# Performance work log

Measured on AMD Instinct MI355X. Metric: run time of the kernel, lower is better.

## Reference

```python
import jax, jax.numpy as jnp
import numpy as np

N_NODES = 50000
N_EDGES = 800000
D_IN = 256
D_HID = 256
D_OUT = 8


def _glorot(key, shape):
    fan_in = shape[-1]
    bound = 1.0 / np.sqrt(fan_in)
    return jax.random.uniform(key, shape, minval=-bound, maxval=bound, dtype=jnp.float32)


def setup_inputs() -> dict:
    key = jax.random.key(0)
    ks = jax.random.split(key, 12)
    x = jax.random.normal(ks[0], (N_NODES, D_IN), dtype=jnp.float32)
    edge_index = jax.random.randint(ks[1], (2, N_EDGES), 0, N_NODES, dtype=jnp.int64)
    return {
        "x": x,
        "edge_index": edge_index,
        # SAGEConv1: lin_l (neighbor path, has bias), lin_r (root path, no bias)
        "W1l": _glorot(ks[2], (D_HID, D_IN)),
        "b1": jnp.zeros((D_HID,), jnp.float32),
        "W1r": _glorot(ks[3], (D_HID, D_IN)),
        # SAGEConv2
        "W2l": _glorot(ks[4], (D_HID, D_HID)),
        "b2": jnp.zeros((D_HID,), jnp.float32),
        "W2r": _glorot(ks[5], (D_HID, D_HID)),
        # MLP decoder
        "Wm1": _glorot(ks[6], (D_HID, D_HID)),
        "bm1": _glorot(ks[7], (D_HID,)),
        "Wm2": _glorot(ks[8], (D_OUT, D_HID)),
        "bm2": _glorot(ks[9], (D_OUT,)),
    }


def _sage_conv(x, edge_index, Wl, b, Wr):
    # PyG SAGEConv with mean aggregation:
    # out = lin_l(mean_{j in N(i)} x_j) + lin_r(x_i)
    src, dst = edge_index[0], edge_index[1]
    msg = x[src]  # [E, d] gather
    agg = jax.ops.segment_sum(msg, dst, num_segments=x.shape[0])  # [N, d]
    cnt = jax.ops.segment_sum(jnp.ones((edge_index.shape[1],), x.dtype), dst,
                              num_segments=x.shape[0])  # in-degree [N]
    mean = agg / jnp.maximum(cnt, 1.0)[:, None]
    return mean @ Wl.T + b + x @ Wr.T


def reference(x, edge_index, W1l, b1, W1r, W2l, b2, W2r, Wm1, bm1, Wm2, bm2):
    h = jax.nn.relu(_sage_conv(x, edge_index, W1l, b1, W1r))
    h = jax.nn.relu(_sage_conv(h, edge_index, W2l, b2, W2r))
    h = jax.nn.relu(h @ Wm1.T + bm1)
    logits = h @ Wm2.T + bm2
    return jax.nn.softmax(logits, axis=-1)
```

## Files before the change

### kernel.cpp

```cpp
#include <hip/hip_runtime.h>
#include <math.h>

#define N_NODES 50000
#define N_EDGES 800000
#define D 256

typedef unsigned short u16;
typedef __attribute__((ext_vector_type(8))) __bf16 bf16x8;
typedef __attribute__((ext_vector_type(4))) float f32x4;

#define BUF_U16 24576
#define NBUF 3

__device__ __forceinline__ void split_hi_lo(float v, u16& h, u16& l) {
    unsigned u = __float_as_uint(v);
    unsigned hh = (u + 0x7fff + ((u >> 16) & 1)) >> 16;
    float hf = __uint_as_float(hh << 16);
    float res = v - hf;
    unsigned ul = __float_as_uint(res);
    unsigned ll = (ul + 0x7fff + ((ul >> 16) & 1)) >> 16;
    h = (u16)hh; l = (u16)ll;
}

__device__ __forceinline__ float bflo(unsigned u) { return __uint_as_float(u << 16); }
__device__ __forceinline__ float bfhi(unsigned u) { return __uint_as_float(u & 0xffff0000u); }

__device__ __forceinline__ void gl_lds16(const void* g, void* l) {
    __builtin_amdgcn_global_load_lds(
        (const __attribute__((address_space(1))) void*)g,
        (__attribute__((address_space(3))) void*)l, 16, 0, 0);
}

__global__ void zero_i32(int* __restrict__ p, int n) {
    int i = blockIdx.x * blockDim.x + threadIdx.x;
    if (i < n) p[i] = 0;
}

__global__ void count_deg(const int* __restrict__ ei, int* __restrict__ cnt) {
    int e = blockIdx.x * blockDim.x + threadIdx.x;
    if (e < N_EDGES) atomicAdd(&cnt[ei[N_EDGES + e]], 1);
}

__global__ void scan1(const int* __restrict__ cnt, int* __restrict__ partial,
                      int* __restrict__ bsum) {
    __shared__ int s[1024];
    int t = threadIdx.x, b = blockIdx.x;
    int gid = b * 1024 + t;
    int v = (gid < N_NODES) ? cnt[gid] : 0;
    s[t] = v;
    __syncthreads();
    for (int off = 1; off < 1024; off <<= 1) {
        int u = (t >= off) ? s[t - off] : 0;
        __syncthreads();
        s[t] += u;
        __syncthreads();
    }
    partial[gid] = s[t];
    if (t == 1023) bsum[b] = s[1023];
}

__global__ void scan2(const int* __restrict__ bsum, int* __restrict__ boff, int nb) {
    int t = threadIdx.x;
    int orig = (t < nb) ? bsum[t] : 0;
    int v = orig;
    #pragma unroll
    for (int off = 1; off < 64; off <<= 1) {
        int u = __shfl_up(v, off, 64);
        if (t >= off) v += u;
    }
    boff[t] = v - orig;
}

__global__ void scan3(const int* __restrict__ partial, const int* __restrict__ boff,
                      int* __restrict__ rowptr, int* __restrict__ cursor) {
    int i = blockIdx.x * blockDim.x + threadIdx.x;
    if (i <= N_NODES) {
        int val = 0;
        if (i > 0) val = partial[i - 1] + boff[(i - 1) >> 10];
        rowptr[i] = val;
        if (i < N_NODES) cursor[i] = val;
    }
}

__global__ void fill_edges(const int* __restrict__ ei, int* __restrict__ cursor,
                           int* __restrict__ esrc) {
    int e = blockIdx.x * blockDim.x + threadIdx.x;
    if (e < N_EDGES) {
        int p = atomicAdd(&cursor[ei[N_EDGES + e]], 1);
        esrc[p] = ei[e];
    }
}

__global__ void split_bf16(const float* __restrict__ in, u16* __restrict__ hi,
                           u16* __restrict__ lo, int n) {
    int i = blockIdx.x * blockDim.x + threadIdx.x;
    if (i < n) {
        u16 h, l; split_hi_lo(in[i], h, l);
        hi[i] = h; lo[i] = l;
    }
}

__global__ __launch_bounds__(256) void aggregate_bf16(const u16* __restrict__ in_hi,
        const int* __restrict__ rowptr, const int* __restrict__ esrc,
        u16* __restrict__ ohi, u16* __restrict__ olo) {
    int node = blockIdx.x * 4 + (threadIdx.x >> 6);
    if (node >= N_NODES) return;
    int lane = threadIdx.x & 63;
    int half = lane >> 5;
    int sub = lane & 31;
    int beg = rowptr[node], end = rowptr[node + 1];
    const u16* rowp = in_hi + sub * 8;

    float a0 = 0.f, a1 = 0.f, a2 = 0.f, a3 = 0.f;
    float a4 = 0.f, a5 = 0.f, a6 = 0.f, a7 = 0.f;

#define ACC8(v) \
    a0 += bflo(v.x); a1 += bfhi(v.x); a2 += bflo(v.y); a3 += bfhi(v.y); \
    a4 += bflo(v.z); a5 += bfhi(v.z); a6 += bflo(v.w); a7 += bfhi(v.w);

    int j = beg;
    for (; j + 16 <= end; j += 16) {
        int i0 = esrc[j +  0 + half];
        int i1 = esrc[j +  2 + half];
        int i2 = esrc[j +  4 + half];
        int i3 = esrc[j +  6 + half];
        int i4 = esrc[j +  8 + half];
        int i5 = esrc[j + 10 + half];
        int i6 = esrc[j + 12 + half];
        int i7 = esrc[j + 14 + half];
        uint4 r0 = *(const uint4*)(rowp + (size_t)i0 * D);
        uint4 r1 = *(const uint4*)(rowp + (size_t)i1 * D);
        uint4 r2 = *(const uint4*)(rowp + (size_t)i2 * D);
        uint4 r3 = *(const uint4*)(rowp + (size_t)i3 * D);
        uint4 r4 = *(const uint4*)(rowp + (size_t)i4 * D);
        uint4 r5 = *(const uint4*)(rowp + (size_t)i5 * D);
        uint4 r6 = *(const uint4*)(rowp + (size_t)i6 * D);
        uint4 r7 = *(const uint4*)(rowp + (size_t)i7 * D);
        ACC8(r0); ACC8(r1); ACC8(r2); ACC8(r3);
        ACC8(r4); ACC8(r5); ACC8(r6); ACC8(r7);
    }
    for (; j + 8 <= end; j += 8) {
        int i0 = esrc[j + 0 + half];
        int i1 = esrc[j + 2 + half];
        int i2 = esrc[j + 4 + half];
        int i3 = esrc[j + 6 + half];
        uint4 r0 = *(const uint4*)(rowp + (size_t)i0 * D);
        uint4 r1 = *(const uint4*)(rowp + (size_t)i1 * D);
        uint4 r2 = *(const uint4*)(rowp + (size_t)i2 * D);
        uint4 r3 = *(const uint4*)(rowp + (size_t)i3 * D);
        ACC8(r0); ACC8(r1); ACC8(r2); ACC8(r3);
    }
    for (; j < end; j += 2) {
        int e = j + half;
        if (e < end) {
            uint4 r = *(const uint4*)(rowp + (size_t)esrc[e] * D);
            ACC8(r);
        }
    }
#undef ACC8

    a0 += __shfl_xor(a0, 32, 64); a1 += __shfl_xor(a1, 32, 64);
    a2 += __shfl_xor(a2, 32, 64); a3 += __shfl_xor(a3, 32, 64);
    a4 += __shfl_xor(a4, 32, 64); a5 += __shfl_xor(a5, 32, 64);
    a6 += __shfl_xor(a6, 32, 64); a7 += __shfl_xor(a7, 32, 64);

    if (lane < 32) {
        float inv = 1.f / (float)max(end - beg, 1);
        float m[8] = { a0 * inv, a1 * inv, a2 * inv, a3 * inv,
                       a4 * inv, a5 * inv, a6 * inv, a7 * inv };
        u16 h[8], l[8];
        #pragma unroll
        for (int k = 0; k < 8; ++k) split_hi_lo(m[k], h[k], l[k]);
        size_t o = (size_t)node * D + lane * 8;
        *(uint4*)(ohi + o) = make_uint4(h[0] | (h[1] << 16), h[2] | (h[3] << 16),
                                        h[4] | (h[5] << 16), h[6] | (h[7] << 16));
        *(uint4*)(olo + o) = make_uint4(l[0] | (l[1] << 16), l[2] | (l[3] << 16),
                                        l[4] | (l[5] << 16), l[6] | (l[7] << 16));
    }
}

__device__ __forceinline__ void stage256(u16* buf,
        const u16* __restrict__ Ah, const u16* __restrict__ Al,
        const u16* __restrict__ Bh, const u16* __restrict__ Bl,
        int ks, int m0, int n0, int t) {
    int tr = t >> 2;
    int g  = (t & 3) ^ ((t >> 3) & 3);
    size_t boff = (size_t)(n0 + tr) * D + ks + g * 8;
    gl_lds16(Bh + boff, buf + 16384 + t * 8);
    gl_lds16(Bl + boff, buf + 20480 + t * 8);
    #pragma unroll
    for (int r = 0; r < 2; ++r) {
        int arow = m0 + r * 128 + tr; if (arow >= N_NODES) arow = N_NODES - 1;
        size_t aoff = (size_t)arow * D + ks + g * 8;
        gl_lds16(Ah + aoff, buf + r * 4096 + t * 8);
        gl_lds16(Al + aoff, buf + 8192 + r * 4096 + t * 8);
    }
}

__global__ __launch_bounds__(512, 1) void gemm_mfma(
        const u16* __restrict__ A1h, const u16* __restrict__ A1l,
        const u16* __restrict__ A2h, const u16* __restrict__ A2l,
        const u16* __restrict__ B1h, const u16* __restrict__ B1l,
        const u16* __restrict__ B2h, const u16* __restrict__ B2l,
        const float* __restrict__ bias, int K, int relu,
        float* __restrict__ Cf, u16* __restrict__ Chi, u16* __restrict__ Clo) {
    extern __shared__ u16 sh[];
    const int t = threadIdx.x;
    const int lane = t & 63;
    const int w = t >> 6;
    const int wm = (w >> 1) * 64, wn = (w & 1) * 64;

    int bid = blockIdx.x;
    int m_idx, n_idx;
    if (bid < 384) {
        m_idx = (bid >> 4) * 8 + (bid & 7);
        n_idx = (bid >> 3) & 1;
    } else {
        int r = bid - 384;
        m_idx = 192 + (r & 3);
        n_idx = r >> 2;
    }
    const int m0 = m_idx * 256, n0 = n_idx * 128;

    f32x4 acc[4][4] = {};

    const int lm = lane & 15;
    const int sw = ((lane >> 4) ^ ((lm >> 1) & 3)) * 8;
    const int nsteps = K >> 5;

    stage256(sh,           A1h, A1l, B1h, B1l,  0, m0, n0, t);
    stage256(sh + BUF_U16, A1h, A1l, B1h, B1l, 32, m0, n0, t);

    int cur = 0;
    for (int s = 0; s < nsteps; ++s) {
        if (s + 1 < nsteps) {
            asm volatile("s_waitcnt vmcnt(6)" ::: "memory");
        } else {
            asm volatile("s_waitcnt vmcnt(0)" ::: "memory");
        }
        __builtin_amdgcn_s_barrier();
        __builtin_amdgcn_sched_barrier(0);

        if (s + 2 < nsteps) {
            int sb = cur + 2; if (sb >= NBUF) sb -= NBUF;
            int ksg = (s + 2) * 32;
            if (ksg < 256) stage256(sh + sb * BUF_U16, A1h, A1l, B1h, B1l, ksg,       m0, n0, t);
            else           stage256(sh + sb * BUF_U16, A2h, A2l, B2h, B2l, ksg - 256, m0, n0, t);
        }

        const u16* buf = sh + cur * BUF_U16;
        bf16x8 ah[4], al[4], bh[4], bl[4];
        #pragma unroll
        for (int i = 0; i < 4; ++i) {
            int offA = (wm + i * 16 + lm) * 32 + sw;
            ah[i] = *(const bf16x8*)(buf + offA);
            al[i] = *(const bf16x8*)(buf + 8192 + offA);
            int offB = (wn + i * 16 + lm) * 32 + sw;
            bh[i] = *(const bf16x8*)(buf + 16384 + offB);
            bl[i] = *(const bf16x8*)(buf + 20480 + offB);
        }
        __builtin_amdgcn_s_setprio(1);
        #pragma unroll
        for (int i = 0; i < 4; ++i) {
            #pragma unroll
            for (int j = 0; j < 4; ++j) {
                acc[i][j] = __builtin_amdgcn_mfma_f32_16x16x32_bf16(ah[i], bh[j], acc[i][j], 0, 0, 0);
                acc[i][j] = __builtin_amdgcn_mfma_f32_16x16x32_bf16(ah[i], bl[j], acc[i][j], 0, 0, 0);
                acc[i][j] = __builtin_amdgcn_mfma_f32_16x16x32_bf16(al[i], bh[j], acc[i][j], 0, 0, 0);
            }
        }
        __builtin_amdgcn_s_setprio(0);

        cur = (cur == NBUF - 1) ? 0 : cur + 1;
    }

    const int q = lane >> 4;
    #pragma unroll
    for (int j = 0; j < 4; ++j) {
        int col = n0 + wn + j * 16 + lm;
        float bb = bias[col];
        #pragma unroll
        for (int i = 0; i < 4; ++i) {
            int rowb = m0 + wm + i * 16 + q * 4;
            #pragma unroll
            for (int r = 0; r < 4; ++r) {
                int row = rowb + r;
                if (row < N_NODES) {
                    float v = acc[i][j][r] + bb;
                    if (relu) v = fmaxf(v, 0.f);
                    size_t o = (size_t)row * D + col;
                    if (Cf) Cf[o] = v;
                    if (Chi) {
                        u16 h, l; split_hi_lo(v, h, l);
                        Chi[o] = h; Clo[o] = l;
                    }
                }
            }
        }
    }
}

__global__ __launch_bounds__(256) void mlp2_softmax(const float* __restrict__ h,
        const float* __restrict__ W, const float* __restrict__ b,
        float* __restrict__ out) {
    int wid = threadIdx.x >> 6;
    int lane = threadIdx.x & 63;
    int n = blockIdx.x * 4 + wid;
    if (n >= N_NODES) return;

    float4 hv = ((const float4*)(h + (size_t)n * D))[lane];
    float acc[8];
    #pragma unroll
    for (int o = 0; o < 8; ++o) {
        float4 w = ((const float4*)(W + o * D))[lane];
        acc[o] = hv.x * w.x + hv.y * w.y + hv.z * w.z + hv.w * w.w;
    }
    #pragma unroll
    for (int o = 0; o < 8; ++o) {
        #pragma unroll
        for (int off = 32; off >= 1; off >>= 1)
            acc[o] += __shfl_xor(acc[o], off, 64);
    }
    if (lane == 0) {
        float v[8];
        float m = -1e30f;
        #pragma unroll
        for (int o = 0; o < 8; ++o) { v[o] = acc[o] + b[o]; m = fmaxf(m, v[o]); }
        float s = 0.f;
        #pragma unroll
        for (int o = 0; o < 8; ++o) { v[o] = expf(v[o] - m); s += v[o]; }
        float inv = 1.f / s;
        float4 o0 = make_float4(v[0] * inv, v[1] * inv, v[2] * inv, v[3] * inv);
        float4 o1 = make_float4(v[4] * inv, v[5] * inv, v[6] * inv, v[7] * inv);
        ((float4*)(out + (size_t)n * 8))[0] = o0;
        ((float4*)(out + (size_t)n * 8))[1] = o1;
    }
}

static inline size_t align_up(size_t x) { return (x + 255) & ~(size_t)255; }

extern "C" void kernel_launch(void* const* d_in, const int* in_sizes, int n_in,
                              void* d_out, int out_size, void* d_ws, size_t ws_size,
                              hipStream_t stream) {
    const float* x   = (const float*)d_in[0];
    const int*   ei  = (const int*)d_in[1];
    const float* W1l = (const float*)d_in[2];
    const float* b1  = (const float*)d_in[3];
    const float* W1r = (const float*)d_in[4];
    const float* W2l = (const float*)d_in[5];
    const float* b2  = (const float*)d_in[6];
    const float* W2r = (const float*)d_in[7];
    const float* Wm1 = (const float*)d_in[8];
    const float* bm1 = (const float*)d_in[9];
    const float* Wm2 = (const float*)d_in[10];
    const float* bm2 = (const float*)d_in[11];
    float* out = (float*)d_out;

    const size_t NF = (size_t)N_NODES * D;
    const size_t NW = (size_t)D * D;

    char* w = (char*)d_ws;
    u16* x_hi  = (u16*)w; w += align_up(NF * 2);
    u16* x_lo  = (u16*)w; w += align_up(NF * 2);
    u16* mn_hi = (u16*)w; w += align_up(NF * 2 * 2);
    u16* mn_lo = mn_hi + NF;
    u16* h1_hi = (u16*)w; w += align_up(NF * 2);
    u16* h1_lo = (u16*)w; w += align_up(NF * 2);
    u16* h2_hi = (u16*)w; w += align_up(NF * 2);
    u16* h2_lo = (u16*)w; w += align_up(NF * 2);
    u16* wbuf  = (u16*)w; w += align_up(NW * 2 * 10);
    u16* w1l_h = wbuf + 0 * NW; u16* w1l_l = wbuf + 1 * NW;
    u16* w1r_h = wbuf + 2 * NW; u16* w1r_l = wbuf + 3 * NW;
    u16* w2l_h = wbuf + 4 * NW; u16* w2l_l = wbuf + 5 * NW;
    u16* w2r_h = wbuf + 6 * NW; u16* w2r_l = wbuf + 7 * NW;
    u16* wm1_h = wbuf + 8 * NW; u16* wm1_l = wbuf + 9 * NW;
    int* cnt     = (int*)w; w += align_up((size_t)N_NODES * 4);
    int* rowptr  = (int*)w; w += align_up((size_t)(N_NODES + 1) * 4);
    int* cursor  = (int*)w; w += align_up((size_t)N_NODES * 4);
    int* partial = (int*)w; w += align_up((size_t)49 * 1024 * 4);
    int* bsum    = (int*)w; w += align_up((size_t)64 * 4);
    int* boff    = (int*)w; w += align_up((size_t)64 * 4);
    int* esrc    = (int*)w; w += align_up((size_t)N_EDGES * 4);
    float* h3 = (float*)mn_hi;

    static bool attr_done = false;
    if (!attr_done) {
        hipFuncSetAttribute((const void*)gemm_mfma,
                            hipFuncAttributeMaxDynamicSharedMemorySize,
                            NBUF * BUF_U16 * 2);
        attr_done = true;
    }

    zero_i32<<<(N_NODES + 255) / 256, 256, 0, stream>>>(cnt, N_NODES);
    count_deg<<<(N_EDGES + 255) / 256, 256, 0, stream>>>(ei, cnt);
    scan1<<<49, 1024, 0, stream>>>(cnt, partial, bsum);
    scan2<<<1, 64, 0, stream>>>(bsum, boff, 49);
    scan3<<<(N_NODES + 256) / 256, 256, 0, stream>>>(partial, boff, rowptr, cursor);
    fill_edges<<<(N_EDGES + 255) / 256, 256, 0, stream>>>(ei, cursor, esrc);

    split_bf16<<<(int)((NF + 255) / 256), 256, 0, stream>>>(x, x_hi, x_lo, (int)NF);
    split_bf16<<<(int)((NW + 255) / 256), 256, 0, stream>>>(W1l, w1l_h, w1l_l, (int)NW);
    split_bf16<<<(int)((NW + 255) / 256), 256, 0, stream>>>(W1r, w1r_h, w1r_l, (int)NW);
    split_bf16<<<(int)((NW + 255) / 256), 256, 0, stream>>>(W2l, w2l_h, w2l_l, (int)NW);
    split_bf16<<<(int)((NW + 255) / 256), 256, 0, stream>>>(W2r, w2r_h, w2r_l, (int)NW);
    split_bf16<<<(int)((NW + 255) / 256), 256, 0, stream>>>(Wm1, wm1_h, wm1_l, (int)NW);

    const int GEMM_LDS = NBUF * BUF_U16 * 2;
    dim3 ggrid(392);
    int agrid = (N_NODES + 3) / 4;

    aggregate_bf16<<<agrid, 256, 0, stream>>>(x_hi, rowptr, esrc, mn_hi, mn_lo);
    gemm_mfma<<<ggrid, 512, GEMM_LDS, stream>>>(mn_hi, mn_lo, x_hi, x_lo,
                                                w1l_h, w1l_l, w1r_h, w1r_l,
                                                b1, 512, 1, nullptr, h1_hi, h1_lo);
    aggregate_bf16<<<agrid, 256, 0, stream>>>(h1_hi, rowptr, esrc, mn_hi, mn_lo);
    gemm_mfma<<<ggrid, 512, GEMM_LDS, stream>>>(mn_hi, mn_lo, h1_hi, h1_lo,
                                                w2l_h, w2l_l, w2r_h, w2r_l,
                                                b2, 512, 1, nullptr, h2_hi, h2_lo);
    gemm_mfma<<<ggrid, 512, GEMM_LDS, stream>>>(h2_hi, h2_lo, h2_hi, h2_lo,
                                                wm1_h, wm1_l, wm1_h, wm1_l,
                                                bm1, 256, 1, h3, nullptr, nullptr);
    mlp2_softmax<<<(N_NODES + 3) / 4, 256, 0, stream>>>(h3, Wm2, bm2, out);
}
```

Measured before the change: 551.0 us.

## Fuse MLP hidden GEMM with output layer and softmax; stage GEMM epilogue through LDS

Replaces the third gemm_mfma launch plus the separate mlp2_softmax kernel with one gemm_mlp2 kernel. It computes a 128x256 tile of the hidden layer, keeps it in LDS, then does the 8-wide output projection and softmax in the same block. This removes the fp32 h3 round trip through global memory and one launch. The conv GEMM epilogue now also writes hi/lo results to LDS first and stores them as coalesced 16-byte vectors instead of scattered 2-byte stores. The cost is an extra barrier and an LDS pass, plus a new kernel that covers full N per block, with fewer blocks (391) and one block per CU.

Result: faster. 519.4 us (-5.7%).

```diff
diff --git a/kernel.cpp b/kernel.cpp
--- a/kernel.cpp
+++ b/kernel.cpp
@@ -202,8 +202,8 @@
         const u16* __restrict__ A2h, const u16* __restrict__ A2l,
         const u16* __restrict__ B1h, const u16* __restrict__ B1l,
         const u16* __restrict__ B2h, const u16* __restrict__ B2l,
-        const float* __restrict__ bias, int K, int relu,
-        float* __restrict__ Cf, u16* __restrict__ Chi, u16* __restrict__ Clo) {
+        const float* __restrict__ bias, int K,
+        u16* __restrict__ Chi, u16* __restrict__ Clo) {
     extern __shared__ u16 sh[];
     const int t = threadIdx.x;
     const int lane = t & 63;
@@ -274,66 +274,168 @@
         cur = (cur == NBUF - 1) ? 0 : cur + 1;
     }
 
+    __syncthreads();
     const int q = lane >> 4;
     #pragma unroll
     for (int j = 0; j < 4; ++j) {
-        int col = n0 + wn + j * 16 + lm;
-        float bb = bias[col];
+        int col = wn + j * 16 + lm;
+        float bb = bias[n0 + col];
         #pragma unroll
         for (int i = 0; i < 4; ++i) {
-            int rowb = m0 + wm + i * 16 + q * 4;
             #pragma unroll
             for (int r = 0; r < 4; ++r) {
-                int row = rowb + r;
-                if (row < N_NODES) {
-                    float v = acc[i][j][r] + bb;
-                    if (relu) v = fmaxf(v, 0.f);
-                    size_t o = (size_t)row * D + col;
-                    if (Cf) Cf[o] = v;
-                    if (Chi) {
-                        u16 h, l; split_hi_lo(v, h, l);
-                        Chi[o] = h; Clo[o] = l;
-                    }
-                }
+                int row = wm + i * 16 + q * 4 + r;
+                float v = fmaxf(acc[i][j][r] + bb, 0.f);
+                u16 h, l; split_hi_lo(v, h, l);
+                sh[row * 128 + col] = h;
+                sh[32768 + row * 128 + col] = l;
             }
         }
     }
-}
-
-__global__ __launch_bounds__(256) void mlp2_softmax(const float* __restrict__ h,
-        const float* __restrict__ W, const float* __restrict__ b,
-        float* __restrict__ out) {
-    int wid = threadIdx.x >> 6;
-    int lane = threadIdx.x & 63;
-    int n = blockIdx.x * 4 + wid;
-    if (n >= N_NODES) return;
-
-    float4 hv = ((const float4*)(h + (size_t)n * D))[lane];
-    float acc[8];
+    __syncthreads();
+    for (int c = t; c < 4096; c += 512) {
+        int row = c >> 4;
+        int off = (c & 15) * 8;
+        int grow = m0 + row;
+        if (grow < N_NODES) {
+            size_t o = (size_t)grow * D + n0 + off;
+            *(uint4*)(Chi + o) = *(const uint4*)(sh + row * 128 + off);
+            *(uint4*)(Clo + o) = *(const uint4*)(sh + 32768 + row * 128 + off);
+        }
+    }
+}
+
+__device__ __forceinline__ void stage_mlp(u16* buf,
+        const u16* __restrict__ Ah, const u16* __restrict__ Al,
+        const u16* __restrict__ Bh, const u16* __restrict__ Bl,
+        int ks, int m0, int t) {
+    int tr = t >> 2;
+    int g  = (t & 3) ^ ((t >> 3) & 3);
+    int arow = m0 + tr; if (arow >= N_NODES) arow = N_NODES - 1;
+    size_t aoff = (size_t)arow * D + ks + g * 8;
+    gl_lds16(Ah + aoff, buf + t * 8);
+    gl_lds16(Al + aoff, buf + 4096 + t * 8);
     #pragma unroll
-    for (int o = 0; o < 8; ++o) {
-        float4 w = ((const float4*)(W + o * D))[lane];
-        acc[o] = hv.x * w.x + hv.y * w.y + hv.z * w.z + hv.w * w.w;
-    }
+    for (int r = 0; r < 2; ++r) {
+        int u = r * 512 + t;
+        int brow = u >> 2;
+        int gb = (u & 3) ^ ((u >> 3) & 3);
+        size_t boff = (size_t)brow * D + ks + gb * 8;
+        gl_lds16(Bh + boff, buf + 8192  + u * 8);
+        gl_lds16(Bl + boff, buf + 16384 + u * 8);
+    }
+}
+
+__global__ __launch_bounds__(512, 1) void gemm_mlp2(
+        const u16* __restrict__ Ah, const u16* __restrict__ Al,
+        const u16* __restrict__ Bh, const u16* __restrict__ Bl,
+        const float* __restrict__ bm1, const float* __restrict__ Wm2,
+        const float* __restrict__ bm2, float* __restrict__ out) {
+    extern __shared__ u16 sh[];
+    const int t = threadIdx.x;
+    const int lane = t & 63;
+    const int w = t >> 6;
+    const int wm = (w >> 2) * 64, wn = (w & 3) * 64;
+    const int m0 = blockIdx.x * 128;
+
+    f32x4 acc[4][4] = {};
+    const int lm = lane & 15;
+    const int sw = ((lane >> 4) ^ ((lm >> 1) & 3)) * 8;
+    const int nsteps = 8;
+
+    stage_mlp(sh,           Ah, Al, Bh, Bl,  0, m0, t);
+    stage_mlp(sh + BUF_U16, Ah, Al, Bh, Bl, 32, m0, t);
+
+    int cur = 0;
+    for (int s = 0; s < nsteps; ++s) {
+        if (s + 1 < nsteps) {
+            asm volatile("s_waitcnt vmcnt(6)" ::: "memory");
+        } else {
+            asm volatile("s_waitcnt vmcnt(0)" ::: "memory");
+        }
+        __builtin_amdgcn_s_barrier();
+        __builtin_amdgcn_sched_barrier(0);
+
+        if (s + 2 < nsteps) {
+            int sb = cur + 2; if (sb >= NBUF) sb -= NBUF;
+            stage_mlp(sh + sb * BUF_U16, Ah, Al, Bh, Bl, (s + 2) * 32, m0, t);
+        }
+
+        const u16* buf = sh + cur * BUF_U16;
+        bf16x8 a_h[4], a_l[4], b_h[4], b_l[4];
+        #pragma unroll
+        for (int i = 0; i < 4; ++i) {
+            int offA = (wm + i * 16 + lm) * 32 + sw;
+            a_h[i] = *(const bf16x8*)(buf + offA);
+            a_l[i] = *(const bf16x8*)(buf + 4096 + offA);
+            int offB = (wn + i * 16 + lm) * 32 + sw;
+            b_h[i] = *(const bf16x8*)(buf + 8192 + offB);
+            b_l[i] = *(const bf16x8*)(buf + 16384 + offB);
+        }
+        __builtin_amdgcn_s_setprio(1);
+        #pragma unroll
+        for (int i = 0; i < 4; ++i) {
+            #pragma unroll
+            for (int j = 0; j < 4; ++j) {
+                acc[i][j] = __builtin_amdgcn_mfma_f32_16x16x32_bf16(a_h[i], b_h[j], acc[i][j], 0, 0, 0);
+                acc[i][j] = __builtin_amdgcn_mfma_f32_16x16x32_bf16(a_h[i], b_l[j], acc[i][j], 0, 0, 0);
+                acc[i][j] = __builtin_amdgcn_mfma_f32_16x16x32_bf16(a_l[i], b_h[j], acc[i][j], 0, 0, 0);
+            }
+        }
+        __builtin_amdgcn_s_setprio(0);
+
+        cur = (cur == NBUF - 1) ? 0 : cur + 1;
+    }
+
+    __syncthreads();
+    float* h3s = (float*)sh;
+    const int q = lane >> 4;
     #pragma unroll
-    for (int o = 0; o < 8; ++o) {
-        #pragma unroll
-        for (int off = 32; off >= 1; off >>= 1)
-            acc[o] += __shfl_xor(acc[o], off, 64);
-    }
-    if (lane == 0) {
-        float v[8];
-        float m = -1e30f;
-        #pragma unroll
-        for (int o = 0; o < 8; ++o) { v[o] = acc[o] + b[o]; m = fmaxf(m, v[o]); }
-        float s = 0.f;
-        #pragma unroll
-        for (int o = 0; o < 8; ++o) { v[o] = expf(v[o] - m); s += v[o]; }
-        float inv = 1.f / s;
-        float4 o0 = make_float4(v[0] * inv, v[1] * inv, v[2] * inv, v[3] * inv);
-        float4 o1 = make_float4(v[4] * inv, v[5] * inv, v[6] * inv, v[7] * inv);
-        ((float4*)(out + (size_t)n * 8))[0] = o0;
-        ((float4*)(out + (size_t)n * 8))[1] = o1;
+    for (int j = 0; j < 4; ++j) {
+        int col = wn + j * 16 + lm;
+        float bb = bm1[col];
+        #pragma unroll
+        for (int i = 0; i < 4; ++i) {
+            #pragma unroll
+            for (int r = 0; r < 4; ++r) {
+                int row = wm + i * 16 + q * 4 + r;
+                h3s[row * 256 + col] = fmaxf(acc[i][j][r] + bb, 0.f);
+            }
+        }
+    }
+    __syncthreads();
+
+    for (int rr = 0; rr < 16; ++rr) {
+        int row = w * 16 + rr;
+        int grow = m0 + row;
+        if (grow >= N_NODES) continue;
+        float4 hv = ((const float4*)(h3s + row * 256))[lane];
+        float a8[8];
+        #pragma unroll
+        for (int o = 0; o < 8; ++o) {
+            float4 wv = ((const float4*)(Wm2 + o * D))[lane];
+            a8[o] = hv.x * wv.x + hv.y * wv.y + hv.z * wv.z + hv.w * wv.w;
+        }
+        #pragma unroll
+        for (int o = 0; o < 8; ++o) {
+            #pragma unroll
+            for (int off = 32; off >= 1; off >>= 1)
+                a8[o] += __shfl_xor(a8[o], off, 64);
+        }
+        if (lane == 0) {
+            float v[8];
+            float mx = -1e30f;
+            #pragma unroll
+            for (int o = 0; o < 8; ++o) { v[o] = a8[o] + bm2[o]; mx = fmaxf(mx, v[o]); }
+            float ssum = 0.f;
+            #pragma unroll
+            for (int o = 0; o < 8; ++o) { v[o] = expf(v[o] - mx); ssum += v[o]; }
+            float inv = 1.f / ssum;
+            float4 o0 = make_float4(v[0] * inv, v[1] * inv, v[2] * inv, v[3] * inv);
+            float4 o1 = make_float4(v[4] * inv, v[5] * inv, v[6] * inv, v[7] * inv);
+            ((float4*)(out + (size_t)grow * 8))[0] = o0;
+            ((float4*)(out + (size_t)grow * 8))[1] = o1;
+        }
     }
 }
 
@@ -381,11 +483,13 @@
     int* bsum    = (int*)w; w += align_up((size_t)64 * 4);
     int* boff    = (int*)w; w += align_up((size_t)64 * 4);
     int* esrc    = (int*)w; w += align_up((size_t)N_EDGES * 4);
-    float* h3 = (float*)mn_hi;
 
     static bool attr_done = false;
     if (!attr_done) {
         hipFuncSetAttribute((const void*)gemm_mfma,
+                            hipFuncAttributeMaxDynamicSharedMemorySize,
+                            NBUF * BUF_U16 * 2);
+        hipFuncSetAttribute((const void*)gemm_mlp2,
                             hipFuncAttributeMaxDynamicSharedMemorySize,
                             NBUF * BUF_U16 * 2);
         attr_done = true;
@@ -412,13 +516,11 @@
     aggregate_bf16<<<agrid, 256, 0, stream>>>(x_hi, rowptr, esrc, mn_hi, mn_lo);
     gemm_mfma<<<ggrid, 512, GEMM_LDS, stream>>>(mn_hi, mn_lo, x_hi, x_lo,
                                                 w1l_h, w1l_l, w1r_h, w1r_l,
-                                                b1, 512, 1, nullptr, h1_hi, h1_lo);
+                                                b1, 512, h1_hi, h1_lo);
     aggregate_bf16<<<agrid, 256, 0, stream>>>(h1_hi, rowptr, esrc, mn_hi, mn_lo);
     gemm_mfma<<<ggrid, 512, GEMM_LDS, stream>>>(mn_hi, mn_lo, h1_hi, h1_lo,
                                                 w2l_h, w2l_l, w2r_h, w2r_l,
-                                                b2, 512, 1, nullptr, h2_hi, h2_lo);
-    gemm_mfma<<<ggrid, 512, GEMM_LDS, stream>>>(h2_hi, h2_lo, h2_hi, h2_lo,
-                                                wm1_h, wm1_l, wm1_h, wm1_l,
-                                                bm1, 256, 1, h3, nullptr, nullptr);
-    mlp2_softmax<<<(N_NODES + 3) / 4, 256, 0, stream>>>(h3, Wm2, bm2, out);
-}
+                                                b2, 512, h2_hi, h2_lo);
+    gemm_mlp2<<<(N_NODES + 127) / 128, 512, GEMM_LDS, stream>>>(
+        h2_hi, h2_lo, wm1_h, wm1_l, bm1, Wm2, bm2, out);
+}
```
